# Performance work log

Hardware: AMD Instinct MI355X
Metric: run time of the kernel (lower is better)

The kernel has to match this reference:

```python
import jax, jax.numpy as jnp
import numpy as np

KERNEL_NUM = 4

def _gaussian_kernels(kernel_size, sigmas, centers):
    # sigmas, centers: [4,1] -> kernels [4,K]; matches torch linspace/exp/normalize
    half = (kernel_size - 1) * 0.5
    xs = jnp.linspace(-half, half, kernel_size)  # [K]
    pdf = jnp.exp(-0.5 * ((xs[None, :] - centers) / (sigmas + 0.001)) ** 2)  # [4,K]
    return pdf / (pdf.sum(axis=1, keepdims=True) + 0.01)


def setup_inputs() -> dict:
    key = jax.random.key(0)
    k1, k2, k3, k4 = jax.random.split(key, 4)
    B, C, L = 4, 512, 2048
    return {
        "x": jax.random.normal(k1, (B, C, L), dtype=jnp.float32),
        "q": jax.random.normal(k2, (B, C, L), dtype=jnp.float32),
        "sigmas": jax.random.uniform(k3, (KERNEL_NUM, 1), dtype=jnp.float32),
        "center_shift": jax.random.uniform(k4, (KERNEL_NUM, 1), dtype=jnp.float32),
        "kernel_size": 7,
    }


def reference(x, q, sigmas, center_shift, kernel_size):
    B, C, L = x.shape
    pad = kernel_size // 2
    # --- 4 gaussian blurs as one grouped conv: same kernel for every channel ---
    kern = _gaussian_kernels(kernel_size, sigmas, center_shift)  # [4,K]
    x_pad = jnp.pad(x, ((0, 0), (0, 0), (pad, pad)), mode='edge')  # replicate pad on L
    lhs = x_pad.reshape(B * C, 1, L + 2 * pad)
    rhs = kern[:, None, :]  # [4,1,K] (cross-correlation, like torch conv1d)
    conv = jax.lax.conv_general_dilated(lhs, rhs, (1,), 'VALID',
                                        dimension_numbers=('NCH', 'OIH', 'NCH'))  # [B*C,4,L]
    x_shift = conv.reshape(B, C, KERNEL_NUM, L).transpose(0, 2, 1, 3)  # [B,4,C,L]
    # --- FFT along channel axis (dim=-2), like torch ---
    qf = jnp.fft.fft(q, axis=-2)[:, None]            # [B,1,C,L] complex
    vf = jnp.fft.fft(x_shift, n=C, axis=-2)          # [B,4,C,L] complex
    # --- complex pearson distance over channel axis ---
    mx = vf.mean(axis=-2, keepdims=True)
    my = qf.mean(axis=-2, keepdims=True)
    dx = vf - mx
    dy = qf - my
    cov = dx * dy
    a = (dx ** 2).sum(axis=-2, keepdims=True)
    b = (dy ** 2).sum(axis=-2, keepdims=True)
    rho = cov / jnp.sqrt(a * b + 1e-4)               # complex
    value_imag = jnp.arctan2(rho.imag, rho.real + 1e-4)
    wm = 2.0 / (1.0 + jnp.exp(-value_imag * 0.5)) - 1.0
    wm = jnp.where(jnp.isnan(wm), 0.0, wm)
    wm = jax.lax.stop_gradient(wm)                   # torch: .clone().detach()
    freq_dist = jnp.abs(vf - qf) ** 2
    w = jnp.exp(-freq_dist * 0.5) * wm               # real [B,4,C,L]
    value_filter = qf * (1.0 - w) + vf * w
    outs = jnp.abs(jnp.fft.ifft(value_filter, n=C, axis=-2))  # [B,4,C,L] real
    # --- softmax channel-attention combine over the 4 kernels ---
    qmean = q.mean(axis=-2)                          # [B,L]
    scores = jnp.einsum('bl,bkcl->bck', qmean, outs)  # [B,C,4]
    wa = jax.nn.softmax(scores, axis=-1)
    return jnp.einsum('bck,bkcl->bcl', wa, outs)      # [B,C,L]
```

## Files before the change

kernel.cpp:

```cpp
#include <hip/hip_runtime.h>
#include <hip/hip_bf16.h>

#define B_DIM 4
#define C_DIM 512
#define L_DIM 2048
#define KN 4
#define MAXKS 9

__device__ inline float bf2f(unsigned short u){ return __uint_as_float(((unsigned)u)<<16); }
__device__ inline unsigned short f2bf(float f){
  unsigned u = __float_as_uint(f);
  unsigned r = (u + 0x7fffu + ((u>>16)&1u))>>16;
  return (unsigned short)r;
}


__device__ __forceinline__ void lane_fft_fwd(float* zr, float* zi,
                                             const float* stw_r, const float* stw_i, int lane){
  #pragma unroll
  for (int s=5; s>=0; --s){
    int m = 1<<s;
    bool hi = (lane & m) != 0;
    float wr = stw_r[s], wi = stw_i[s];
    #pragma unroll
    for (int j=0;j<8;++j){
      float pr = __shfl_xor(zr[j], m);
      float pi = __shfl_xor(zi[j], m);
      float sr = hi ? (pr - zr[j]) : (zr[j] + pr);
      float si = hi ? (pi - zi[j]) : (zi[j] + pi);
      float mr = sr*wr - si*wi;
      float mi = sr*wi + si*wr;
      zr[j] = hi ? mr : sr;
      zi[j] = hi ? mi : si;
    }
  }
}

__device__ __forceinline__ void lane_fft_inv(float* zr, float* zi,
                                             const float* stw_r, const float* stw_i, int lane){
  #pragma unroll
  for (int s=0; s<6; ++s){
    int m = 1<<s;
    bool hi = (lane & m) != 0;
    float wr = stw_r[s], wi = -stw_i[s];
    #pragma unroll
    for (int j=0;j<8;++j){
      float pr = __shfl_xor(zr[j], m);
      float pi = __shfl_xor(zi[j], m);
      float ar = hi ? zr[j] : pr;
      float ai = hi ? zi[j] : pi;
      float mr = ar*wr - ai*wi;
      float mi = ar*wi + ai*wr;
      zr[j] = hi ? (pr - mr) : (zr[j] + mr);
      zi[j] = hi ? (pi - mi) : (zi[j] + mi);
    }
  }
}

__device__ __forceinline__ void fft8_reg(float* zr, float* zi, float sgn){
  const float C = 0.70710678118654752f;
  float s0r=zr[0]+zr[4], s0i=zi[0]+zi[4];
  float s1r=zr[0]-zr[4], s1i=zi[0]-zi[4];
  float s2r=zr[2]+zr[6], s2i=zi[2]+zi[6];
  float s3r=zr[2]-zr[6], s3i=zi[2]-zi[6];
  float e0r=s0r+s2r, e0i=s0i+s2i;
  float e2r=s0r-s2r, e2i=s0i-s2i;
  float j3r=-sgn*s3i, j3i=sgn*s3r;
  float e1r=s1r+j3r, e1i=s1i+j3i;
  float e3r=s1r-j3r, e3i=s1i-j3i;
  float t0r=zr[1]+zr[5], t0i=zi[1]+zi[5];
  float t1r=zr[1]-zr[5], t1i=zi[1]-zi[5];
  float t2r=zr[3]+zr[7], t2i=zi[3]+zi[7];
  float t3r=zr[3]-zr[7], t3i=zi[3]-zi[7];
  float o0r=t0r+t2r, o0i=t0i+t2i;
  float o2r=t0r-t2r, o2i=t0i-t2i;
  float k3r=-sgn*t3i, k3i=sgn*t3r;
  float o1r=t1r+k3r, o1i=t1i+k3i;
  float o3r=t1r-k3r, o3i=t1i-k3i;
  float w1o_r = C*o1r - sgn*C*o1i;
  float w1o_i = C*o1i + sgn*C*o1r;
  float w2o_r = -sgn*o2i, w2o_i = sgn*o2r;
  float w3o_r = -C*o3r - sgn*C*o3i;
  float w3o_i = -C*o3i + sgn*C*o3r;
  zr[0]=e0r+o0r;   zi[0]=e0i+o0i;
  zr[4]=e0r-o0r;   zi[4]=e0i-o0i;
  zr[1]=e1r+w1o_r; zi[1]=e1i+w1o_i;
  zr[5]=e1r-w1o_r; zi[5]=e1i-w1o_i;
  zr[2]=e2r+w2o_r; zi[2]=e2i+w2o_i;
  zr[6]=e2r-w2o_r; zi[6]=e2i-w2o_i;
  zr[3]=e3r+w3o_r; zi[3]=e3i+w3o_i;
  zr[7]=e3r-w3o_r; zi[7]=e3i-w3o_i;
}

__device__ __forceinline__ void fft512_fwd(float* zr, float* zi,
    const float* stw_r, const float* stw_i,
    const float* btw_r, const float* btw_i, int lane){
  lane_fft_fwd(zr, zi, stw_r, stw_i, lane);
  #pragma unroll
  for (int j=1;j<8;++j){
    float ar=zr[j], ai=zi[j];
    zr[j]=ar*btw_r[j]-ai*btw_i[j];
    zi[j]=ar*btw_i[j]+ai*btw_r[j];
  }
  fft8_reg(zr, zi, -1.f);
}

__device__ __forceinline__ void fft512_inv(float* zr, float* zi,
    const float* stw_r, const float* stw_i,
    const float* btw_r, const float* btw_i, int lane){
  fft8_reg(zr, zi, +1.f);
  #pragma unroll
  for (int j=1;j<8;++j){
    float ar=zr[j], ai=zi[j];
    zr[j]= ar*btw_r[j]+ai*btw_i[j];
    zi[j]=-ar*btw_i[j]+ai*btw_r[j];
  }
  lane_fft_inv(zr, zi, stw_r, stw_i, lane);
}

__device__ __forceinline__ void wreduce4(float&a,float&b,float&c,float&d){
  #pragma unroll
  for (int off=1; off<64; off<<=1){
    a += __shfl_xor(a,off); b += __shfl_xor(b,off);
    c += __shfl_xor(c,off); d += __shfl_xor(d,off);
  }
}

__global__ __launch_bounds__(256) void col_kernel(
    const float* __restrict__ x, const float* __restrict__ q,
    const float* __restrict__ sigmas, const float* __restrict__ centers,
    const int* __restrict__ ksp,
    unsigned short* __restrict__ outs, float* __restrict__ qmean)
{
  __shared__ float kern[KN][MAXKS];
  int tid  = threadIdx.x;
  int wave = tid >> 6;
  int lane = tid & 63;
  int col  = blockIdx.x*4 + wave;
  int b = col >> 11;
  int l = col & 2047;
  int ks  = ksp[0];
  int pad = ks >> 1;

  if (tid < KN){
    float half = 0.5f*(float)(ks-1);
    float sg = sigmas[tid] + 0.001f;
    float ce = centers[tid];
    float s = 0.f;
    for (int t=0;t<ks;++t){ float d=((float)t-half-ce)/sg; s += expf(-0.5f*d*d); }
    float inv = 1.f/(s+0.01f);
    for (int t=0;t<ks;++t){ float d=((float)t-half-ce)/sg; kern[tid][t] = expf(-0.5f*d*d)*inv; }
  }
  __syncthreads();

  const float PI = 3.14159265358979323846f;
  int k1 = (int)(__brev((unsigned)lane) >> 26);

  float stw_r[6], stw_i[6];
  #pragma unroll
  for (int s=0; s<6; ++s){
    int m = 1<<s;
    float ang = -PI * (float)(lane & (m-1)) / (float)m;
    float sn, cs; sincosf(ang, &sn, &cs);
    stw_r[s]=cs; stw_i[s]=sn;
  }
  float btw_r[8], btw_i[8];
  #pragma unroll
  for (int j=0;j<8;++j){
    float ang = -2.f*PI*(float)(j*k1)/512.f;
    float sn, cs; sincosf(ang, &sn, &cs);
    btw_r[j]=cs; btw_i[j]=sn;
  }

  float qre[8], qim[8];
  const float* qbase = q + ((size_t)(b*512) + lane*8)*2048 + l;
  #pragma unroll
  for (int j=0;j<8;++j){ qre[j] = qbase[(size_t)j*2048]; qim[j]=0.f; }

  float cv[KN][8];
  #pragma unroll
  for (int k=0;k<KN;++k){
    #pragma unroll
    for (int j=0;j<8;++j) cv[k][j]=0.f;
  }
  const float* xbase = x + ((size_t)(b*512) + lane*8)*2048;
  for (int t=0;t<ks;++t){
    int li = l + t - pad;
    li = li<0 ? 0 : (li>2047 ? 2047 : li);
    float xv[8];
    #pragma unroll
    for (int j=0;j<8;++j) xv[j] = xbase[(size_t)j*2048 + li];
    #pragma unroll
    for (int k=0;k<KN;++k){
      float w = kern[k][t];
      #pragma unroll
      for (int j=0;j<8;++j) cv[k][j] += w*xv[j];
    }
  }

  fft512_fwd(qre,qim,stw_r,stw_i,btw_r,btw_i,lane);
  if (lane==0) qmean[b*2048+l] = qre[0]*(1.f/512.f);

  float S1r=0.f,S1i=0.f,S2r=0.f,S2i=0.f;
  #pragma unroll
  for (int j=0;j<8;++j){
    S1r += qre[j]; S1i += qim[j];
    S2r += qre[j]*qre[j]-qim[j]*qim[j];
    S2i += 2.f*qre[j]*qim[j];
  }
  wreduce4(S1r,S1i,S2r,S2i);
  float myr = S1r*(1.f/512.f), myi = S1i*(1.f/512.f);
  float bsr = S2r - (S1r*myr - S1i*myi);
  float bsi = S2i - (S1r*myi + S1i*myr);

  #pragma unroll
  for (int k=0;k<KN;++k){
    float vr[8], vi[8];
    #pragma unroll
    for (int j=0;j<8;++j){ vr[j]=cv[k][j]; vi[j]=0.f; }
    fft512_fwd(vr,vi,stw_r,stw_i,btw_r,btw_i,lane);

    float T1r=0.f,T1i=0.f,T2r=0.f,T2i=0.f;
    #pragma unroll
    for (int j=0;j<8;++j){
      T1r += vr[j]; T1i += vi[j];
      T2r += vr[j]*vr[j]-vi[j]*vi[j];
      T2i += 2.f*vr[j]*vi[j];
    }
    wreduce4(T1r,T1i,T2r,T2i);
    float mxr = T1r*(1.f/512.f), mxi = T1i*(1.f/512.f);
    float asr = T2r - (T1r*mxr - T1i*mxi);
    float asi = T2i - (T1r*mxi + T1i*mxr);
    float zr_ = asr*bsr - asi*bsi + 1.0e-4f;
    float zi_ = asr*bsi + asi*bsr;
    float rmag = sqrtf(zr_*zr_+zi_*zi_);
    float dr = sqrtf(fmaxf(0.5f*(rmag+zr_),0.f));
    float di = sqrtf(fmaxf(0.5f*(rmag-zr_),0.f));
    di = (zi_ < 0.f) ? -di : di;
    float den = dr*dr + di*di;
    float invr = 0.f, invi = 0.f;
    if (den > 0.f){ invr = dr/den; invi = -di/den; }

    #pragma unroll
    for (int j=0;j<8;++j){
      float vr_=vr[j], vi_=vi[j], qr_=qre[j], qi_=qim[j];
      float dxr = vr_-mxr, dxi = vi_-mxi;
      float dyr = qr_-myr, dyi = qi_-myi;
      float cvr = dxr*dyr - dxi*dyi;
      float cvi = dxr*dyi + dxi*dyr;
      float rr = cvr*invr - cvi*invi;
      float ri = cvr*invi + cvi*invr;
      float ang = atan2f(ri, rr + 1.0e-4f);
      float wm  = tanhf(ang*0.25f);
      if (!(wm==wm)) wm = 0.f;
      float fdr = vr_-qr_, fdi = vi_-qi_;
      float w = expf(-0.5f*(fdr*fdr+fdi*fdi))*wm;
      vr[j] = qr_ + w*fdr;
      vi[j] = qi_ + w*fdi;
    }

    fft512_inv(vr,vi,stw_r,stw_i,btw_r,btw_i,lane);

    size_t obase = ((size_t)((b*KN+k)*2048 + l))*512 + lane*8;
    unsigned short ob[8];
    #pragma unroll
    for (int j=0;j<8;++j){
      float mag = sqrtf(vr[j]*vr[j]+vi[j]*vi[j])*(1.f/512.f);
      ob[j] = f2bf(mag);
    }
    uint4 pk;
    pk.x = (unsigned)ob[0] | ((unsigned)ob[1]<<16);
    pk.y = (unsigned)ob[2] | ((unsigned)ob[3]<<16);
    pk.z = (unsigned)ob[4] | ((unsigned)ob[5]<<16);
    pk.w = (unsigned)ob[6] | ((unsigned)ob[7]<<16);
    *reinterpret_cast<uint4*>(outs + obase) = pk;
  }
}

__global__ __launch_bounds__(256) void scores_kernel(
    const unsigned short* __restrict__ outs, const float* __restrict__ qmean,
    float* __restrict__ scores)
{
  int tid = threadIdx.x;
  int l0 = blockIdx.x*128;
  int k = blockIdx.y;
  int b = blockIdx.z;
  int c = tid*2;
  float accx=0.f, accy=0.f;
  for (int l=l0; l<l0+128; ++l){
    float s = qmean[b*2048+l];
    const unsigned short* p = outs + ((size_t)((b*KN+k)*2048 + l))*512 + c;
    unsigned int u = *(const unsigned int*)p;
    accx += s*bf2f((unsigned short)(u&0xffffu));
    accy += s*bf2f((unsigned short)(u>>16));
  }
  atomicAdd(&scores[(size_t)(b*512+c)*KN + k], accx);
  atomicAdd(&scores[(size_t)(b*512+c+1)*KN + k], accy);
}

__global__ __launch_bounds__(256) void combine_kernel(
    const unsigned short* __restrict__ outs, const float* __restrict__ scores,
    float* __restrict__ out)
{
  __shared__ float wa[64][KN];
  int cx = threadIdx.x;
  int ly = threadIdx.y;
  int l0 = blockIdx.x*64;
  int c  = blockIdx.y*64 + cx;
  int b  = blockIdx.z;
  if (ly==0){
    float4 s = *reinterpret_cast<const float4*>(&scores[(size_t)(b*512+c)*KN]);
    float m = fmaxf(fmaxf(s.x,s.y),fmaxf(s.z,s.w));
    float e0=expf(s.x-m), e1=expf(s.y-m), e2=expf(s.z-m), e3=expf(s.w-m);
    float inv = 1.f/(e0+e1+e2+e3);
    wa[cx][0]=e0*inv; wa[cx][1]=e1*inv; wa[cx][2]=e2*inv; wa[cx][3]=e3*inv;
  }
  __syncthreads();
  float acc[16];
  #pragma unroll
  for (int i=0;i<16;++i) acc[i]=0.f;
  for (int k=0;k<KN;++k){
    float w = wa[cx][k];
    const unsigned short* p = outs + ((size_t)((b*KN+k)*2048) + l0 + ly*16)*512 + c;
    #pragma unroll
    for (int i=0;i<16;++i){
      acc[i] += w*bf2f(p[(size_t)i*512]);
    }
  }
  float* op = out + ((size_t)(b*512+c))*2048 + l0 + ly*16;
  #pragma unroll
  for (int i=0;i<16;i+=4){
    float4 v = make_float4(acc[i],acc[i+1],acc[i+2],acc[i+3]);
    *reinterpret_cast<float4*>(op+i) = v;
  }
}

extern "C" void kernel_launch(void* const* d_in, const int* in_sizes, int n_in,
                              void* d_out, int out_size, void* d_ws, size_t ws_size,
                              hipStream_t stream)
{
  const float* x   = (const float*)d_in[0];
  const float* q   = (const float*)d_in[1];
  const float* sig = (const float*)d_in[2];
  const float* cen = (const float*)d_in[3];
  const int*   ksp = (const int*)d_in[4];
  float* out = (float*)d_out;

  unsigned short* outs = (unsigned short*)d_ws;
  size_t outs_elems = (size_t)B_DIM*KN*L_DIM*C_DIM;
  float* qmeanb = (float*)((char*)d_ws + outs_elems*sizeof(unsigned short));
  float* scores = qmeanb + (size_t)B_DIM*L_DIM;

  hipMemsetAsync(scores, 0, (size_t)B_DIM*C_DIM*KN*sizeof(float), stream);

  dim3 g1(B_DIM*L_DIM/4);
  hipLaunchKernelGGL(col_kernel, g1, dim3(256), 0, stream,
                     x, q, sig, cen, ksp, outs, qmeanb);
  dim3 g2(L_DIM/128, KN, B_DIM);
  hipLaunchKernelGGL(scores_kernel, g2, dim3(256), 0, stream, outs, qmeanb, scores);
  dim3 g3(L_DIM/64, C_DIM/64, B_DIM);
  hipLaunchKernelGGL(combine_kernel, g3, dim3(64,4), 0, stream, outs, scores, out);
}
```

Measured before the change: 276.9 us.

## Pack real FFT pairs into complex FFTs and use fast transcendentals

Real-input forward FFTs are packed in pairs into single complex 512-point FFTs (q with kernel 0, kernels 1 and 2) and split apart with a cross-lane shuffle. This cuts the forward transforms from five to three. atan2, tanh, exp and the twiddle sincos calls are replaced with polynomial and intrinsic approximations, and launch bounds now ask for 3 blocks per CU. The trade is lower accuracy from the approximations and possible register pressure under the occupancy hint.

```diff
diff --git a/kernel.cpp b/kernel.cpp
--- a/kernel.cpp
+++ b/kernel.cpp
@@ -14,6 +14,20 @@
   return (unsigned short)r;
 }
 
+__device__ __forceinline__ float fast_atan2(float y, float x){
+  float ax = fabsf(x), ay = fabsf(y);
+  float mx = fmaxf(ax, ay), mn = fminf(ax, ay);
+  float t = __fdividef(mn, mx);
+  float a = t*t;
+  float r = t*(0.9998660f + a*(-0.3302995f + a*(0.1801410f + a*(-0.0851330f + a*0.0208351f))));
+  r = (ay > ax) ? 1.5707963267948966f - r : r;
+  r = (x < 0.f) ? 3.14159265358979323846f - r : r;
+  return copysignf(r, y);
+}
+__device__ __forceinline__ float fast_tanh(float u){
+  float e = exp2f(2.8853900817779268f*u);
+  return __fdividef(e-1.f, e+1.f);
+}
 
 __device__ __forceinline__ void lane_fft_fwd(float* zr, float* zi,
                                              const float* stw_r, const float* stw_i, int lane){
@@ -118,6 +132,23 @@
   lane_fft_inv(zr, zi, stw_r, stw_i, lane);
 }
 
+__device__ __forceinline__ void rfft_separate(const float* zr, const float* zi,
+    float* ar, float* ai, float* br, float* bi, int plane, int lane){
+  #pragma unroll
+  for (int j=0;j<8;++j){
+    const int js = 7-j;
+    const int j0 = (8-j)&7;
+    float pr = __shfl(zr[js], plane);
+    float pi = __shfl(zi[js], plane);
+    pr = (lane==0) ? zr[j0] : pr;
+    pi = (lane==0) ? zi[j0] : pi;
+    ar[j] = 0.5f*(zr[j]+pr);
+    ai[j] = 0.5f*(zi[j]-pi);
+    br[j] = 0.5f*(zi[j]+pi);
+    bi[j] = 0.5f*(pr-zr[j]);
+  }
+}
+
 __device__ __forceinline__ void wreduce4(float&a,float&b,float&c,float&d){
   #pragma unroll
   for (int off=1; off<64; off<<=1){
@@ -126,7 +157,71 @@
   }
 }
 
-__global__ __launch_bounds__(256) void col_kernel(
+__device__ __forceinline__ void process_k(float* vr, float* vi,
+    const float* qre, const float* qim,
+    float myr, float myi, float bsr, float bsi,
+    const float* stw_r, const float* stw_i,
+    const float* btw_r, const float* btw_i,
+    int lane, unsigned short* outp)
+{
+  float T1r=0.f,T1i=0.f,T2r=0.f,T2i=0.f;
+  #pragma unroll
+  for (int j=0;j<8;++j){
+    T1r += vr[j]; T1i += vi[j];
+    T2r += vr[j]*vr[j]-vi[j]*vi[j];
+    T2i += 2.f*vr[j]*vi[j];
+  }
+  wreduce4(T1r,T1i,T2r,T2i);
+  float mxr = T1r*(1.f/512.f), mxi = T1i*(1.f/512.f);
+  float asr = T2r - (T1r*mxr - T1i*mxi);
+  float asi = T2i - (T1r*mxi + T1i*mxr);
+  float zr_ = asr*bsr - asi*bsi + 1.0e-4f;
+  float zi_ = asr*bsi + asi*bsr;
+  float rmag = sqrtf(zr_*zr_+zi_*zi_);
+  float dr = sqrtf(fmaxf(0.5f*(rmag+zr_),0.f));
+  float di = sqrtf(fmaxf(0.5f*(rmag-zr_),0.f));
+  di = (zi_ < 0.f) ? -di : di;
+  float den = dr*dr + di*di;
+  float invden = __fdividef(1.f, den);
+  float invr = (den>0.f) ? dr*invden : 0.f;
+  float invi = (den>0.f) ? -di*invden : 0.f;
+
+  #pragma unroll
+  for (int j=0;j<8;++j){
+    float vr_=vr[j], vi_=vi[j], qr_=qre[j], qi_=qim[j];
+    float dxr = vr_-mxr, dxi = vi_-mxi;
+    float dyr = qr_-myr, dyi = qi_-myi;
+    float cvr = dxr*dyr - dxi*dyi;
+    float cvi = dxr*dyi + dxi*dyr;
+    float rr = cvr*invr - cvi*invi;
+    float ri = cvr*invi + cvi*invr;
+    float ang = fast_atan2(ri, rr + 1.0e-4f);
+    float wm  = fast_tanh(ang*0.25f);
+    if (!(wm==wm)) wm = 0.f;
+    float fdr = vr_-qr_, fdi = vi_-qi_;
+    float fd2 = fdr*fdr+fdi*fdi;
+    float w = exp2f(-0.72134752044448170f*fd2)*wm;
+    vr[j] = qr_ + w*fdr;
+    vi[j] = qi_ + w*fdi;
+  }
+
+  fft512_inv(vr,vi,stw_r,stw_i,btw_r,btw_i,lane);
+
+  unsigned short ob[8];
+  #pragma unroll
+  for (int j=0;j<8;++j){
+    float mag = sqrtf(vr[j]*vr[j]+vi[j]*vi[j])*(1.f/512.f);
+    ob[j] = f2bf(mag);
+  }
+  uint4 pk;
+  pk.x = (unsigned)ob[0] | ((unsigned)ob[1]<<16);
+  pk.y = (unsigned)ob[2] | ((unsigned)ob[3]<<16);
+  pk.z = (unsigned)ob[4] | ((unsigned)ob[5]<<16);
+  pk.w = (unsigned)ob[6] | ((unsigned)ob[7]<<16);
+  *reinterpret_cast<uint4*>(outp) = pk;
+}
+
+__global__ __launch_bounds__(256,3) void col_kernel(
     const float* __restrict__ x, const float* __restrict__ q,
     const float* __restrict__ sigmas, const float* __restrict__ centers,
     const int* __restrict__ ksp,
@@ -155,50 +250,46 @@
 
   const float PI = 3.14159265358979323846f;
   int k1 = (int)(__brev((unsigned)lane) >> 26);
+  int plane; { int pk_ = (64-k1)&63; plane = (int)(__brev((unsigned)pk_)>>26); }
 
   float stw_r[6], stw_i[6];
   #pragma unroll
   for (int s=0; s<6; ++s){
     int m = 1<<s;
     float ang = -PI * (float)(lane & (m-1)) / (float)m;
-    float sn, cs; sincosf(ang, &sn, &cs);
-    stw_r[s]=cs; stw_i[s]=sn;
+    stw_r[s]=__cosf(ang); stw_i[s]=__sinf(ang);
   }
   float btw_r[8], btw_i[8];
   #pragma unroll
   for (int j=0;j<8;++j){
     float ang = -2.f*PI*(float)(j*k1)/512.f;
-    float sn, cs; sincosf(ang, &sn, &cs);
-    btw_r[j]=cs; btw_i[j]=sn;
-  }
-
-  float qre[8], qim[8];
+    btw_r[j]=__cosf(ang); btw_i[j]=__sinf(ang);
+  }
+
+  float qv[8];
   const float* qbase = q + ((size_t)(b*512) + lane*8)*2048 + l;
   #pragma unroll
-  for (int j=0;j<8;++j){ qre[j] = qbase[(size_t)j*2048]; qim[j]=0.f; }
-
-  float cv[KN][8];
-  #pragma unroll
-  for (int k=0;k<KN;++k){
-    #pragma unroll
-    for (int j=0;j<8;++j) cv[k][j]=0.f;
-  }
+  for (int j=0;j<8;++j) qv[j] = qbase[(size_t)j*2048];
+
+  float c0[8], c1[8], c2[8], c3[8];
+  #pragma unroll
+  for (int j=0;j<8;++j){ c0[j]=0.f; c1[j]=0.f; c2[j]=0.f; c3[j]=0.f; }
   const float* xbase = x + ((size_t)(b*512) + lane*8)*2048;
   for (int t=0;t<ks;++t){
     int li = l + t - pad;
     li = li<0 ? 0 : (li>2047 ? 2047 : li);
-    float xv[8];
+    float w0=kern[0][t], w1=kern[1][t], w2=kern[2][t], w3=kern[3][t];
     #pragma unroll
-    for (int j=0;j<8;++j) xv[j] = xbase[(size_t)j*2048 + li];
-    #pragma unroll
-    for (int k=0;k<KN;++k){
-      float w = kern[k][t];
-      #pragma unroll
-      for (int j=0;j<8;++j) cv[k][j] += w*xv[j];
+    for (int j=0;j<8;++j){
+      float xv = xbase[(size_t)j*2048 + li];
+      c0[j] += w0*xv; c1[j] += w1*xv; c2[j] += w2*xv; c3[j] += w3*xv;
     }
   }
 
-  fft512_fwd(qre,qim,stw_r,stw_i,btw_r,btw_i,lane);
+  fft512_fwd(qv, c0, stw_r,stw_i,btw_r,btw_i, lane);
+  float qre[8], qim[8], vr[8], vi[8];
+  rfft_separate(qv, c0, qre, qim, vr, vi, plane, lane);
+
   if (lane==0) qmean[b*2048+l] = qre[0]*(1.f/512.f);
 
   float S1r=0.f,S1i=0.f,S2r=0.f,S2i=0.f;
@@ -213,68 +304,22 @@
   float bsr = S2r - (S1r*myr - S1i*myi);
   float bsi = S2i - (S1r*myi + S1i*myr);
 
-  #pragma unroll
-  for (int k=0;k<KN;++k){
-    float vr[8], vi[8];
-    #pragma unroll
-    for (int j=0;j<8;++j){ vr[j]=cv[k][j]; vi[j]=0.f; }
-    fft512_fwd(vr,vi,stw_r,stw_i,btw_r,btw_i,lane);
-
-    float T1r=0.f,T1i=0.f,T2r=0.f,T2i=0.f;
-    #pragma unroll
-    for (int j=0;j<8;++j){
-      T1r += vr[j]; T1i += vi[j];
-      T2r += vr[j]*vr[j]-vi[j]*vi[j];
-      T2i += 2.f*vr[j]*vi[j];
-    }
-    wreduce4(T1r,T1i,T2r,T2i);
-    float mxr = T1r*(1.f/512.f), mxi = T1i*(1.f/512.f);
-    float asr = T2r - (T1r*mxr - T1i*mxi);
-    float asi = T2i - (T1r*mxi + T1i*mxr);
-    float zr_ = asr*bsr - asi*bsi + 1.0e-4f;
-    float zi_ = asr*bsi + asi*bsr;
-    float rmag = sqrtf(zr_*zr_+zi_*zi_);
-    float dr = sqrtf(fmaxf(0.5f*(rmag+zr_),0.f));
-    float di = sqrtf(fmaxf(0.5f*(rmag-zr_),0.f));
-    di = (zi_ < 0.f) ? -di : di;
-    float den = dr*dr + di*di;
-    float invr = 0.f, invi = 0.f;
-    if (den > 0.f){ invr = dr/den; invi = -di/den; }
-
-    #pragma unroll
-    for (int j=0;j<8;++j){
-      float vr_=vr[j], vi_=vi[j], qr_=qre[j], qi_=qim[j];
-      float dxr = vr_-mxr, dxi = vi_-mxi;
-      float dyr = qr_-myr, dyi = qi_-myi;
-      float cvr = dxr*dyr - dxi*dyi;
-      float cvi = dxr*dyi + dxi*dyr;
-      float rr = cvr*invr - cvi*invi;
-      float ri = cvr*invi + cvi*invr;
-      float ang = atan2f(ri, rr + 1.0e-4f);
-      float wm  = tanhf(ang*0.25f);
-      if (!(wm==wm)) wm = 0.f;
-      float fdr = vr_-qr_, fdi = vi_-qi_;
-      float w = expf(-0.5f*(fdr*fdr+fdi*fdi))*wm;
-      vr[j] = qr_ + w*fdr;
-      vi[j] = qi_ + w*fdi;
-    }
-
-    fft512_inv(vr,vi,stw_r,stw_i,btw_r,btw_i,lane);
-
-    size_t obase = ((size_t)((b*KN+k)*2048 + l))*512 + lane*8;
-    unsigned short ob[8];
-    #pragma unroll
-    for (int j=0;j<8;++j){
-      float mag = sqrtf(vr[j]*vr[j]+vi[j]*vi[j])*(1.f/512.f);
-      ob[j] = f2bf(mag);
-    }
-    uint4 pk;
-    pk.x = (unsigned)ob[0] | ((unsigned)ob[1]<<16);
-    pk.y = (unsigned)ob[2] | ((unsigned)ob[3]<<16);
-    pk.z = (unsigned)ob[4] | ((unsigned)ob[5]<<16);
-    pk.w = (unsigned)ob[6] | ((unsigned)ob[7]<<16);
-    *reinterpret_cast<uint4*>(outs + obase) = pk;
-  }
+  size_t obase = ((size_t)((b*KN)*2048 + l))*512 + lane*8;
+  const size_t kstride = (size_t)2048*512;
+
+  process_k(vr, vi, qre,qim, myr,myi,bsr,bsi, stw_r,stw_i,btw_r,btw_i, lane,
+            outs + obase);
+  fft512_fwd(c1, c2, stw_r,stw_i,btw_r,btw_i, lane);
+  rfft_separate(c1, c2, qv, c0, vr, vi, plane, lane);
+  process_k(qv, c0, qre,qim, myr,myi,bsr,bsi, stw_r,stw_i,btw_r,btw_i, lane,
+            outs + obase + kstride);
+  process_k(vr, vi, qre,qim, myr,myi,bsr,bsi, stw_r,stw_i,btw_r,btw_i, lane,
+            outs + obase + 2*kstride);
+  #pragma unroll
+  for (int j=0;j<8;++j) c2[j]=0.f;
+  fft512_fwd(c3, c2, stw_r,stw_i,btw_r,btw_i, lane);
+  process_k(c3, c2, qre,qim, myr,myi,bsr,bsi, stw_r,stw_i,btw_r,btw_i, lane,
+            outs + obase + 3*kstride);
 }
 
 __global__ __launch_bounds__(256) void scores_kernel(
```

Measured after the change: 250.2 us. 9.6% less time.
